# Performance work log

Measured on AMD Instinct MI355X. Metric: run time of the kernel, lower is better.

## Reference

```python
import jax, jax.numpy as jnp
import numpy as np

HIDDEN = 1024
BATCH = 4
SEQ = 2048

def setup_inputs() -> dict:
    key = jax.random.key(0)
    ks = jax.random.split(key, 4)
    scale = 1.0 / np.sqrt(HIDDEN)
    return {
        "X": jax.random.normal(ks[0], (BATCH, SEQ, HIDDEN), dtype=jnp.float32),
        "Wq": jax.random.normal(ks[1], (HIDDEN, HIDDEN), dtype=jnp.float32) * scale,
        "bq": jnp.zeros((HIDDEN,), dtype=jnp.float32),
        "Wk": jax.random.normal(ks[2], (HIDDEN, HIDDEN), dtype=jnp.float32) * scale,
        "bk": jnp.zeros((HIDDEN,), dtype=jnp.float32),
        "Wv": jax.random.normal(ks[3], (HIDDEN, HIDDEN), dtype=jnp.float32) * scale,
        "bv": jnp.zeros((HIDDEN,), dtype=jnp.float32),
    }

def reference(X, Wq, bq, Wk, bk, Wv, bv):
    # q,k,v: [B, S, H]; nn.Linear computes x @ W^T + b
    q = jnp.einsum('bsh,oh->bso', X, Wq) + bq
    k = jnp.einsum('bsh,oh->bso', X, Wk) + bk
    v = jnp.einsum('bsh,oh->bso', X, Wv) + bv
    hidden_dim = X.shape[-1]
    # scores: [B, S, S]
    scores = jnp.einsum('bqh,bkh->bqk', q, k) / jnp.sqrt(jnp.float32(hidden_dim))
    attn = jax.nn.softmax(scores, axis=-1)  # dropout p=0 (eval reference)
    return jnp.einsum('bqk,bkh->bqh', attn, v)
```

## Files before the change

kernel.cpp:

```cpp
#include <hip/hip_runtime.h>
#include <hip/hip_bf16.h>
#include <cstdint>

typedef __bf16 bf16_t;
typedef __bf16 bf16x8 __attribute__((ext_vector_type(8)));
typedef float f32x4 __attribute__((ext_vector_type(4)));

__device__ __forceinline__ void g2lds16(const bf16_t* g, bf16_t* l) {
  __builtin_amdgcn_global_load_lds(
      (const __attribute__((address_space(1))) uint32_t*)g,
      (__attribute__((address_space(3))) uint32_t*)l, 16, 0, 0);
}

__global__ __launch_bounds__(256) void cast_f32_bf16(const float* __restrict__ src,
                                                     bf16_t* __restrict__ dst, int n8) {
  int i = blockIdx.x * 256 + threadIdx.x;
  if (i >= n8) return;
  const float4* s4 = reinterpret_cast<const float4*>(src);
  float4 a = s4[2 * i], b = s4[2 * i + 1];
  bf16x8 o;
  o[0] = (bf16_t)a.x; o[1] = (bf16_t)a.y; o[2] = (bf16_t)a.z; o[3] = (bf16_t)a.w;
  o[4] = (bf16_t)b.x; o[5] = (bf16_t)b.y; o[6] = (bf16_t)b.z; o[7] = (bf16_t)b.w;
  reinterpret_cast<bf16x8*>(dst)[i] = o;
}

__global__ __launch_bounds__(256) void softmax_rows(bf16_t* __restrict__ P) {
  const int t = threadIdx.x, lane = t & 63, wave = t >> 6;
  bf16_t* p = P + (long)blockIdx.x * 2048;
  bf16x8 v = reinterpret_cast<bf16x8*>(p)[t];
  float f[8];
  #pragma unroll
  for (int e = 0; e < 8; e++) f[e] = (float)v[e];
  float m = f[0];
  #pragma unroll
  for (int e = 1; e < 8; e++) m = fmaxf(m, f[e]);
  #pragma unroll
  for (int o = 32; o > 0; o >>= 1) m = fmaxf(m, __shfl_xor(m, o));
  __shared__ float red[4];
  if (lane == 0) red[wave] = m;
  __syncthreads();
  m = fmaxf(fmaxf(red[0], red[1]), fmaxf(red[2], red[3]));
  float s = 0.f;
  #pragma unroll
  for (int e = 0; e < 8; e++) { f[e] = __expf(f[e] - m); s += f[e]; }
  #pragma unroll
  for (int o = 32; o > 0; o >>= 1) s += __shfl_xor(s, o);
  __syncthreads();
  if (lane == 0) red[wave] = s;
  __syncthreads();
  s = red[0] + red[1] + red[2] + red[3];
  const float inv = 1.0f / s;
  #pragma unroll
  for (int e = 0; e < 8; e++) v[e] = (bf16_t)(f[e] * inv);
  reinterpret_cast<bf16x8*>(p)[t] = v;
}

template<int MODE>
__global__ __launch_bounds__(512, 2) void gemm8p(
    const bf16_t* __restrict__ A, const bf16_t* __restrict__ B,
    int lda, int ldb, int K, int ldo,
    long sAz, long sBz, long sOz,
    bf16_t* __restrict__ o_q, bf16_t* __restrict__ o_k, bf16_t* __restrict__ o_vt,
    const float* __restrict__ bqp, const float* __restrict__ bkp, const float* __restrict__ bvp,
    bf16_t* __restrict__ o_s, float scale, float* __restrict__ o_f)
{
  __shared__ bf16_t As[2][16384];
  __shared__ bf16_t Bs[2][16384];
  const int t = threadIdx.x;
  const int lane = t & 63;
  const int wave = t >> 6;
  const int wr = wave >> 2, wc = wave & 3;
  const int m0 = blockIdx.y * 256, n0 = blockIdx.x * 256;
  const int bz = blockIdx.z;
  A += (long)bz * sAz;
  B += (long)bz * sBz;

  const int srow = t >> 3;
  const int scolB = (((t & 7) << 4) ^ ((srow & 7) << 4));
  const bf16_t* Abase = A + (long)m0 * lda + (scolB >> 1);
  const bf16_t* Bbase = B + (long)n0 * ldb + (scolB >> 1);

  const int laneRow = lane & 15;
  const int laneK16 = (lane >> 4) << 4;
  const int rflip = (laneRow & 7) << 4;
  const char* AsB = (const char*)&As[0][0];
  const char* BsB = (const char*)&Bs[0][0];

  f32x4 acc[8][4];
  #pragma unroll
  for (int i = 0; i < 8; ++i)
    #pragma unroll
    for (int j = 0; j < 4; ++j) { f32x4 z = {0.f, 0.f, 0.f, 0.f}; acc[i][j] = z; }

#define STAGE_A(bb, h, kt) do { \
    const bf16_t* _s = Abase + (long)((h) * 128 + srow) * lda + (kt) * 64; \
    g2lds16(_s, &As[bb][(h) * 8192 + t * 8]); \
    g2lds16(_s + (long)64 * lda, &As[bb][(h) * 8192 + 4096 + t * 8]); \
  } while (0)
#define STAGE_B(bb, h, kt) do { \
    const bf16_t* _s = Bbase + (long)((h) * 128 + srow) * ldb + (kt) * 64; \
    g2lds16(_s, &Bs[bb][(h) * 8192 + t * 8]); \
    g2lds16(_s + (long)64 * ldb, &Bs[bb][(h) * 8192 + 4096 + t * 8]); \
  } while (0)

  bf16x8 a[4][2], b[2][2];

#define LOADA(mh, bc) do { \
    _Pragma("unroll") \
    for (int fi2 = 0; fi2 < 4; ++fi2) { \
      const int row = (mh) * 128 + wr * 64 + fi2 * 16 + laneRow; \
      _Pragma("unroll") \
      for (int ks = 0; ks < 2; ++ks) { \
        const int off = ((bc) * 32768 + (row << 7) + (ks << 6) + laneK16) ^ rflip; \
        a[fi2][ks] = *reinterpret_cast<const bf16x8*>(AsB + off); \
      } \
    } \
  } while (0)
#define LOADB(nh, bc) do { \
    _Pragma("unroll") \
    for (int fj2 = 0; fj2 < 2; ++fj2) { \
      const int row = (nh) * 128 + wc * 32 + fj2 * 16 + laneRow; \
      _Pragma("unroll") \
      for (int ks = 0; ks < 2; ++ks) { \
        const int off = ((bc) * 32768 + (row << 7) + (ks << 6) + laneK16) ^ rflip; \
        b[fj2][ks] = *reinterpret_cast<const bf16x8*>(BsB + off); \
      } \
    } \
  } while (0)
#define QUAD(mh, nh) do { \
    _Pragma("unroll") \
    for (int fi2 = 0; fi2 < 4; ++fi2) \
      _Pragma("unroll") \
      for (int ks = 0; ks < 2; ++ks) \
        _Pragma("unroll") \
        for (int fj2 = 0; fj2 < 2; ++fj2) \
          acc[(mh) * 4 + fi2][(nh) * 2 + fj2] = __builtin_amdgcn_mfma_f32_16x16x32_bf16( \
              a[fi2][ks], b[fj2][ks], acc[(mh) * 4 + fi2][(nh) * 2 + fj2], 0, 0, 0); \
  } while (0)
#define PH_MID() do { \
    __builtin_amdgcn_s_barrier(); \
    asm volatile("s_waitcnt lgkmcnt(0)" ::: "memory"); \
    __builtin_amdgcn_sched_barrier(0); \
    __builtin_amdgcn_s_setprio(1); \
  } while (0)
#define PH_END() do { \
    __builtin_amdgcn_s_setprio(0); \
    __builtin_amdgcn_s_barrier(); \
  } while (0)
#define PH_ENDV() do { \
    __builtin_amdgcn_s_setprio(0); \
    asm volatile("s_waitcnt vmcnt(4)" ::: "memory"); \
    __builtin_amdgcn_s_barrier(); \
  } while (0)

  const int NT = K >> 6;
  const int NITER = K >> 7;

  STAGE_A(0, 0, 0);
  STAGE_B(0, 0, 0);
  STAGE_A(0, 1, 0);
  STAGE_B(0, 1, 0);
  STAGE_A(1, 0, 1);
  STAGE_B(1, 0, 1);
  asm volatile("s_waitcnt vmcnt(4)" ::: "memory");
  __builtin_amdgcn_s_barrier();

  for (int it = 0; it < NITER; ++it) {
    const int T1 = 2 * it + 1;
    int T2 = 2 * it + 2; if (T2 >= NT) T2 = NT - 1;
    int T3 = 2 * it + 3; if (T3 >= NT) T3 = NT - 1;
    LOADA(0, 0); LOADB(0, 0);
    STAGE_A(1, 1, T1);
    PH_MID(); QUAD(0, 0); PH_END();
    LOADB(1, 0);
    STAGE_B(1, 1, T1);
    PH_MID(); QUAD(0, 1); PH_END();
    LOADA(1, 0); LOADB(0, 0);
    STAGE_A(0, 0, T2);
    PH_MID(); QUAD(1, 0); PH_END();
    LOADB(1, 0);
    STAGE_B(0, 0, T2);
    PH_MID(); QUAD(1, 1); PH_ENDV();
    LOADA(0, 1); LOADB(0, 1);
    STAGE_A(0, 1, T2);
    PH_MID(); QUAD(0, 0); PH_END();
    LOADB(1, 1);
    STAGE_B(0, 1, T2);
    PH_MID(); QUAD(0, 1); PH_END();
    LOADA(1, 1); LOADB(0, 1);
    STAGE_A(1, 0, T3);
    PH_MID(); QUAD(1, 0); PH_END();
    LOADB(1, 1);
    STAGE_B(1, 0, T3);
    PH_MID(); QUAD(1, 1); PH_ENDV();
  }

  const int er = (lane >> 4) << 2;
  const int ec = lane & 15;
  #pragma unroll
  for (int mh = 0; mh < 2; ++mh)
  #pragma unroll
  for (int fi2 = 0; fi2 < 4; ++fi2) {
    const int mg = m0 + mh * 128 + wr * 64 + fi2 * 16 + er;
    #pragma unroll
    for (int nh = 0; nh < 2; ++nh)
    #pragma unroll
    for (int fj2 = 0; fj2 < 2; ++fj2) {
      const int ng = n0 + nh * 128 + wc * 32 + fj2 * 16 + ec;
      const f32x4 v = acc[mh * 4 + fi2][nh * 2 + fj2];
      if constexpr (MODE == 0) {
        if (ng < 1024) {
          const float bb = bqp[ng];
          #pragma unroll
          for (int r = 0; r < 4; ++r)
            o_q[(long)(mg + r) * 1024 + ng] = (bf16_t)(v[r] + bb);
        } else if (ng < 2048) {
          const int nn = ng - 1024;
          const float bb = bkp[nn];
          #pragma unroll
          for (int r = 0; r < 4; ++r)
            o_k[(long)(mg + r) * 1024 + nn] = (bf16_t)(v[r] + bb);
        } else {
          const int nn = ng - 2048;
          const float bb = bvp[nn];
          const int bat = mg >> 11, sr = mg & 2047;
          union { bf16_t h[4]; uint2 u; } pk;
          #pragma unroll
          for (int r = 0; r < 4; ++r) pk.h[r] = (bf16_t)(v[r] + bb);
          *reinterpret_cast<uint2*>(&o_vt[((long)bat * 1024 + nn) * 2048 + sr]) = pk.u;
        }
      } else if constexpr (MODE == 1) {
        bf16_t* os = o_s + (long)bz * sOz;
        #pragma unroll
        for (int r = 0; r < 4; ++r)
          os[(long)(mg + r) * ldo + ng] = (bf16_t)(v[r] * scale);
      } else {
        float* of = o_f + (long)bz * sOz;
        #pragma unroll
        for (int r = 0; r < 4; ++r)
          of[(long)(mg + r) * ldo + ng] = v[r];
      }
    }
  }
#undef STAGE_A
#undef STAGE_B
#undef LOADA
#undef LOADB
#undef QUAD
#undef PH_MID
#undef PH_END
#undef PH_ENDV
}

extern "C" void kernel_launch(void* const* d_in, const int* in_sizes, int n_in,
                              void* d_out, int out_size, void* d_ws, size_t ws_size,
                              hipStream_t stream) {
  const float* X  = (const float*)d_in[0];
  const float* Wq = (const float*)d_in[1];
  const float* bq = (const float*)d_in[2];
  const float* Wk = (const float*)d_in[3];
  const float* bk = (const float*)d_in[4];
  const float* Wv = (const float*)d_in[5];
  const float* bv = (const float*)d_in[6];
  float* out = (float*)d_out;

  constexpr long SEG = 16777216;
  char* ws = (char*)d_ws;
  bf16_t* Q  = (bf16_t*)(ws + 0 * SEG);
  bf16_t* Kc = (bf16_t*)(ws + 1 * SEG);
  bf16_t* Vt = (bf16_t*)(ws + 2 * SEG);
  bf16_t* Xb = (bf16_t*)(ws + 3 * SEG);
  bf16_t* Wc = (bf16_t*)(ws + 4 * SEG);
  bf16_t* P  = (bf16_t*)(ws + 3 * SEG);

  cast_f32_bf16<<<4096, 256, 0, stream>>>(X,  Xb, 1048576);
  cast_f32_bf16<<<512,  256, 0, stream>>>(Wq, Wc,           131072);
  cast_f32_bf16<<<512,  256, 0, stream>>>(Wk, Wc + 1048576, 131072);
  cast_f32_bf16<<<512,  256, 0, stream>>>(Wv, Wc + 2097152, 131072);

  dim3 blk(512);
  {
    dim3 g(3072 / 256, 8192 / 256, 1);
    gemm8p<0><<<g, blk, 0, stream>>>(Xb, Wc, 1024, 1024, 1024, 1024, 0, 0, 0,
                                     Q, Kc, Vt, bq, bk, bv, nullptr, 0.f, nullptr);
  }
  {
    dim3 g(2048 / 256, 2048 / 256, 4);
    gemm8p<1><<<g, blk, 0, stream>>>(Q, Kc, 1024, 1024, 1024, 2048,
                                     2097152, 2097152, 4194304,
                                     nullptr, nullptr, nullptr, nullptr, nullptr, nullptr,
                                     P, 0.03125f, nullptr);
  }
  softmax_rows<<<8192, 256, 0, stream>>>(P);
  {
    dim3 g(1024 / 256, 2048 / 256, 4);
    gemm8p<2><<<g, blk, 0, stream>>>(P, Vt, 2048, 2048, 2048, 1024,
                                     4194304, 2097152, 2097152,
                                     nullptr, nullptr, nullptr, nullptr, nullptr, nullptr,
                                     nullptr, 0.f, out);
  }
}
```

Measured before the change: 199.2 us.

## Add dedicated 128x256 triple-buffered GEMM kernel for P·V stage

```diff
diff --git a/kernel.cpp b/kernel.cpp
--- a/kernel.cpp
+++ b/kernel.cpp
@@ -229,16 +229,11 @@
           for (int r = 0; r < 4; ++r) pk.h[r] = (bf16_t)(v[r] + bb);
           *reinterpret_cast<uint2*>(&o_vt[((long)bat * 1024 + nn) * 2048 + sr]) = pk.u;
         }
-      } else if constexpr (MODE == 1) {
+      } else {
         bf16_t* os = o_s + (long)bz * sOz;
         #pragma unroll
         for (int r = 0; r < 4; ++r)
           os[(long)(mg + r) * ldo + ng] = (bf16_t)(v[r] * scale);
-      } else {
-        float* of = o_f + (long)bz * sOz;
-        #pragma unroll
-        for (int r = 0; r < 4; ++r)
-          of[(long)(mg + r) * ldo + ng] = v[r];
       }
     }
   }
@@ -250,6 +245,146 @@
 #undef PH_MID
 #undef PH_END
 #undef PH_ENDV
+}
+
+__global__ __launch_bounds__(512, 2) void gemm128pv(
+    const bf16_t* __restrict__ A, const bf16_t* __restrict__ B,
+    int lda, int ldb, int K, int ldo,
+    long sAz, long sBz, long sOz, float* __restrict__ o_f)
+{
+  __shared__ bf16_t As3[3][8192];
+  __shared__ bf16_t Bs3[3][16384];
+  const int t = threadIdx.x;
+  const int lane = t & 63;
+  const int wave = t >> 6;
+  const int wr = wave >> 2, wc = wave & 3;
+  const int m0 = blockIdx.y * 128, n0 = blockIdx.x * 256;
+  const int bz = blockIdx.z;
+  A += (long)bz * sAz;
+  B += (long)bz * sBz;
+
+  const int srow = t >> 3;
+  const int scolB = (((t & 7) << 4) ^ ((srow & 7) << 4));
+  const bf16_t* Abase = A + (long)m0 * lda + (scolB >> 1);
+  const bf16_t* Bbase = B + (long)n0 * ldb + (scolB >> 1);
+
+  const int laneRow = lane & 15;
+  const int laneK16 = (lane >> 4) << 4;
+  const int rflip = (laneRow & 7) << 4;
+  const char* AsB = (const char*)&As3[0][0];
+  const char* BsB = (const char*)&Bs3[0][0];
+
+  f32x4 acc[4][4];
+  #pragma unroll
+  for (int i = 0; i < 4; ++i)
+    #pragma unroll
+    for (int j = 0; j < 4; ++j) { f32x4 z = {0.f, 0.f, 0.f, 0.f}; acc[i][j] = z; }
+
+#define PSTAGE_A(se, kt) do { \
+    const bf16_t* _s = Abase + (long)srow * lda + (kt) * 64; \
+    g2lds16(_s, &As3[0][0] + (se) + t * 8); \
+    g2lds16(_s + (long)64 * lda, &As3[0][0] + (se) + 4096 + t * 8); \
+  } while (0)
+#define PSTAGE_B(se, h, kt) do { \
+    const bf16_t* _s = Bbase + (long)((h) * 128 + srow) * ldb + (kt) * 64; \
+    g2lds16(_s, &Bs3[0][0] + (se) + (h) * 8192 + t * 8); \
+    g2lds16(_s + (long)64 * ldb, &Bs3[0][0] + (se) + (h) * 8192 + 4096 + t * 8); \
+  } while (0)
+
+  bf16x8 a[4][2], b[2][2];
+
+#define PLOADA(cAb) do { \
+    _Pragma("unroll") \
+    for (int fi2 = 0; fi2 < 4; ++fi2) { \
+      const int row = wr * 64 + fi2 * 16 + laneRow; \
+      _Pragma("unroll") \
+      for (int ks = 0; ks < 2; ++ks) { \
+        const int off = (cAb) + (((row << 7) + (ks << 6) + laneK16) ^ rflip); \
+        a[fi2][ks] = *reinterpret_cast<const bf16x8*>(AsB + off); \
+      } \
+    } \
+  } while (0)
+#define PLOADB(nh, cBb) do { \
+    _Pragma("unroll") \
+    for (int fj2 = 0; fj2 < 2; ++fj2) { \
+      const int row = (nh) * 128 + wc * 32 + fj2 * 16 + laneRow; \
+      _Pragma("unroll") \
+      for (int ks = 0; ks < 2; ++ks) { \
+        const int off = (cBb) + (((row << 7) + (ks << 6) + laneK16) ^ rflip); \
+        b[fj2][ks] = *reinterpret_cast<const bf16x8*>(BsB + off); \
+      } \
+    } \
+  } while (0)
+#define PQUAD(nh) do { \
+    _Pragma("unroll") \
+    for (int fi2 = 0; fi2 < 4; ++fi2) \
+      _Pragma("unroll") \
+      for (int ks = 0; ks < 2; ++ks) \
+        _Pragma("unroll") \
+        for (int fj2 = 0; fj2 < 2; ++fj2) \
+          acc[fi2][(nh) * 2 + fj2] = __builtin_amdgcn_mfma_f32_16x16x32_bf16( \
+              a[fi2][ks], b[fj2][ks], acc[fi2][(nh) * 2 + fj2], 0, 0, 0); \
+  } while (0)
+#define PPH_MID() do { \
+    __builtin_amdgcn_s_barrier(); \
+    asm volatile("s_waitcnt lgkmcnt(0)" ::: "memory"); \
+    __builtin_amdgcn_sched_barrier(0); \
+    __builtin_amdgcn_s_setprio(1); \
+  } while (0)
+
+  const int NT = K >> 6;
+
+  PSTAGE_A(0, 0);      PSTAGE_B(0, 0, 0);      PSTAGE_B(0, 1, 0);
+  PSTAGE_A(8192, 1);   PSTAGE_B(16384, 0, 1);  PSTAGE_B(16384, 1, 1);
+  asm volatile("s_waitcnt vmcnt(6)" ::: "memory");
+  __builtin_amdgcn_s_barrier();
+
+  int cAb = 0, cBb = 0;
+  int sAe = 16384, sBe = 32768;
+
+  for (int T = 0; T < NT; ++T) {
+    int Tp2 = T + 2; if (Tp2 >= NT) Tp2 = NT - 1;
+    PLOADA(cAb); PLOADB(0, cBb);
+    PSTAGE_A(sAe, Tp2);
+    PSTAGE_B(sBe, 0, Tp2);
+    PPH_MID(); PQUAD(0);
+    __builtin_amdgcn_s_setprio(0);
+    __builtin_amdgcn_s_barrier();
+    PLOADB(1, cBb);
+    PSTAGE_B(sBe, 1, Tp2);
+    PPH_MID(); PQUAD(1);
+    __builtin_amdgcn_s_setprio(0);
+    asm volatile("s_waitcnt vmcnt(6)" ::: "memory");
+    __builtin_amdgcn_s_barrier();
+    cAb = (cAb == 32768) ? 0 : cAb + 16384;
+    cBb = (cBb == 65536) ? 0 : cBb + 32768;
+    sAe = (sAe == 16384) ? 0 : sAe + 8192;
+    sBe = (sBe == 32768) ? 0 : sBe + 16384;
+  }
+
+  const int er = (lane >> 4) << 2;
+  const int ec = lane & 15;
+  float* of = o_f + (long)bz * sOz;
+  #pragma unroll
+  for (int fi2 = 0; fi2 < 4; ++fi2) {
+    const int mg = m0 + wr * 64 + fi2 * 16 + er;
+    #pragma unroll
+    for (int nh = 0; nh < 2; ++nh)
+    #pragma unroll
+    for (int fj2 = 0; fj2 < 2; ++fj2) {
+      const int ng = n0 + nh * 128 + wc * 32 + fj2 * 16 + ec;
+      const f32x4 v = acc[fi2][nh * 2 + fj2];
+      #pragma unroll
+      for (int r = 0; r < 4; ++r)
+        of[(long)(mg + r) * ldo + ng] = v[r];
+    }
+  }
+#undef PSTAGE_A
+#undef PSTAGE_B
+#undef PLOADA
+#undef PLOADB
+#undef PQUAD
+#undef PPH_MID
 }
 
 extern "C" void kernel_launch(void* const* d_in, const int* in_sizes, int n_in,
@@ -293,10 +428,8 @@
   }
   softmax_rows<<<8192, 256, 0, stream>>>(P);
   {
-    dim3 g(1024 / 256, 2048 / 256, 4);
-    gemm8p<2><<<g, blk, 0, stream>>>(P, Vt, 2048, 2048, 2048, 1024,
-                                     4194304, 2097152, 2097152,
-                                     nullptr, nullptr, nullptr, nullptr, nullptr, nullptr,
-                                     nullptr, 0.f, out);
-  }
-}
+    dim3 g(1024 / 256, 2048 / 128, 4);
+    gemm128pv<<<g, blk, 0, stream>>>(P, Vt, 2048, 2048, 2048, 1024,
+                                     4194304, 2097152, 2097152, out);
+  }
+}
```

Result: faster. 186.4 us (-6.4%).
